# Performance work log

Measured on AMD Instinct MI355X. Metric: run time of the kernel, lower is better.

The kernel has to match this reference:

```python
import jax, jax.numpy as jnp
import numpy as np

EMBED = 1024
HEADS = 16
HEAD_DIM = EMBED // HEADS
FF = 4096
EPS = 1e-5


def layer_norm(x, g, b):
    mu = jnp.mean(x, axis=-1, keepdims=True)
    var = jnp.mean(jnp.square(x - mu), axis=-1, keepdims=True)
    return (x - mu) * jax.lax.rsqrt(var + EPS) * g + b


def setup_inputs() -> dict:
    key = jax.random.key(0)
    ks = jax.random.split(key, 16)
    s = 0.02
    x = jax.random.normal(ks[0], (4, 2048, EMBED), dtype=jnp.float32)
    d = {
        "x": x,
        "Wq": jax.random.normal(ks[1], (EMBED, EMBED), jnp.float32) * s,
        "bq": jnp.zeros((EMBED,), jnp.float32),
        "Wk": jax.random.normal(ks[2], (EMBED, EMBED), jnp.float32) * s,
        "bk": jnp.zeros((EMBED,), jnp.float32),
        "Wv": jax.random.normal(ks[3], (EMBED, EMBED), jnp.float32) * s,
        "bv": jnp.zeros((EMBED,), jnp.float32),
        "Wo": jax.random.normal(ks[4], (EMBED, EMBED), jnp.float32) * s,
        "bo": jnp.zeros((EMBED,), jnp.float32),
        "W1": jax.random.normal(ks[5], (EMBED, FF), jnp.float32) * s,
        "b1": jnp.zeros((FF,), jnp.float32),
        "W2": jax.random.normal(ks[6], (FF, EMBED), jnp.float32) * s,
        "b2": jnp.zeros((EMBED,), jnp.float32),
        "ln1_g": jnp.ones((EMBED,), jnp.float32),
        "ln1_b": jnp.zeros((EMBED,), jnp.float32),
        "ln2_g": jnp.ones((EMBED,), jnp.float32),
        "ln2_b": jnp.zeros((EMBED,), jnp.float32),
    }
    return d


def reference(x, Wq, bq, Wk, bk, Wv, bv, Wo, bo, W1, b1, W2, b2, ln1_g, ln1_b, ln2_g, ln2_b):
    B, S, E = x.shape
    scale = np.sqrt(HEAD_DIM).astype(np.float32)
    # project and split heads: (B, H, S, Dh)
    def heads(t):
        return t.reshape(B, S, HEADS, HEAD_DIM).transpose(0, 2, 1, 3)
    Q = heads(x @ Wq + bq)
    K = heads(x @ Wk + bk)
    V = heads(x @ Wv + bv)
    scores = jnp.einsum("bhqd,bhkd->bhqk", Q, K) / scale
    attn = jax.nn.softmax(scores, axis=-1)
    ctx = jnp.einsum("bhqk,bhkd->bhqd", attn, V)
    ctx = ctx.transpose(0, 2, 1, 3).reshape(B, S, E)
    attn_out = ctx @ Wo + bo
    x = layer_norm(x + attn_out, ln1_g, ln1_b)
    ff = jax.nn.relu(x @ W1 + b1) @ W2 + b2
    x = layer_norm(x + ff, ln2_g, ln2_b)
    return x
```

## Files before the change

kernel.cpp:

```cpp
#include <hip/hip_runtime.h>
#include <stdint.h>

typedef uint16_t u16;
typedef __bf16 bf16x8 __attribute__((ext_vector_type(8)));
typedef float f32x4 __attribute__((ext_vector_type(4)));

__device__ __forceinline__ float bf2f(u16 u) {
  union { uint32_t i; float f; } v; v.i = ((uint32_t)u) << 16; return v.f;
}
__device__ __forceinline__ u16 f2bf(float f) {
  union { float f; uint32_t i; } v; v.f = f;
  uint32_t r = v.i + 0x7fffu + ((v.i >> 16) & 1u);
  return (u16)(r >> 16);
}
__device__ __forceinline__ uint32_t pack2(float a, float b) {
  return (uint32_t)f2bf(a) | ((uint32_t)f2bf(b) << 16);
}
__device__ __forceinline__ void gll16(const u16* g, u16* l) {
  __builtin_amdgcn_global_load_lds((const __attribute__((address_space(1))) void*)g,
                                   (__attribute__((address_space(3))) void*)l, 16, 0, 0);
}

__global__ __launch_bounds__(256) void f32_to_bf16(
    const float* __restrict__ in, u16* __restrict__ out)
{
  int idx = blockIdx.x * 256 + threadIdx.x;
  float4 v = *(const float4*)(in + (size_t)idx * 4);
  uint2 o;
  o.x = pack2(v.x, v.y);
  o.y = pack2(v.z, v.w);
  *(uint2*)(out + (size_t)idx * 4) = o;
}

__global__ __launch_bounds__(256) void concat_bias(
    const float* __restrict__ a, const float* __restrict__ b,
    const float* __restrict__ c, float* __restrict__ o)
{
  int i = blockIdx.x * 256 + threadIdx.x;
  float v = (i < 1024) ? a[i] : ((i < 2048) ? b[i - 1024] : c[i - 2048]);
  o[i] = v;
}

__global__ __launch_bounds__(256) void transpose_f2b(
    const float* __restrict__ in, u16* __restrict__ out, int R, int C, int ldo)
{
  __shared__ u16 tile[32][33];
  int c0 = blockIdx.x * 32, r0 = blockIdx.y * 32;
  int x = threadIdx.x, y = threadIdx.y;
#pragma unroll
  for (int i = 0; i < 32; i += 8)
    tile[y + i][x] = f2bf(in[(size_t)(r0 + y + i) * C + (c0 + x)]);
  __syncthreads();
#pragma unroll
  for (int i = 0; i < 32; i += 8)
    out[(size_t)(c0 + y + i) * ldo + (r0 + x)] = tile[x][y + i];
}

__global__ __launch_bounds__(256) void transpose_v(
    const u16* __restrict__ src, u16* __restrict__ dst)
{
  __shared__ u16 tile[64][72];
  int kc = blockIdx.x;
  int bh = blockIdx.y;
  int b = bh >> 4, h = bh & 15;
  int t = threadIdx.x;
  int r = t >> 3;
  int c0 = (t & 7) * 8;
  const u16* s0 = src + ((size_t)(b * 2048 + kc * 64 + r) * 3072) + h * 64 + c0;
#pragma unroll
  for (int hh = 0; hh < 2; hh++)
    *(uint4*)(&tile[r + hh * 32][c0]) = *(const uint4*)(s0 + (size_t)hh * 32 * 3072);
  __syncthreads();
#pragma unroll
  for (int hh = 0; hh < 2; hh++) {
    int d = r + hh * 32;
    u16 vals[8];
#pragma unroll
    for (int p = 0; p < 8; p++) {
      int pos = c0 + p;
      int key = ((pos & 3) << 4) | ((pos >> 2) & 15);
      vals[p] = tile[key][d];
    }
    *(uint4*)(dst + ((size_t)bh * 64 + d) * 2048 + (size_t)kc * 64 + c0) = *(uint4*)vals;
  }
}

#define BM 128
#define BN 128
#define BK 64

__global__ __launch_bounds__(256, 2) void gemm_bt(
    const u16* __restrict__ A, const u16* __restrict__ BT,
    const float* __restrict__ bias, u16* __restrict__ C,
    int N, int K, int lda, int ldb, int ldc, int relu, int addC)
{
  __shared__ __align__(16) u16 As[BM][BK];
  __shared__ __align__(16) u16 Bs[BN][BK];
  int tid = threadIdx.x;
  int gx = gridDim.x;
  int id = blockIdx.y * gx + blockIdx.x;
  int cpx = (gx * gridDim.y) >> 3;
  int nid = (id & 7) * cpx + (id >> 3);
  int m0 = (nid / gx) * BM, n0 = (nid % gx) * BN;
  int wave = tid >> 6, lane = tid & 63;
  int quad = lane >> 4, tr = lane & 15;
  int wm = (wave >> 1) * 64, wn = (wave & 1) * 64;
  int tr7 = tr & 7;

  f32x4 zero = {0.f, 0.f, 0.f, 0.f};
  f32x4 acc[4][4];
#pragma unroll
  for (int i = 0; i < 4; i++)
#pragma unroll
    for (int j = 0; j < 4; j++) acc[i][j] = zero;

  int srow = tid >> 3;
  int sblk = (tid & 7) ^ (srow & 7);
  const u16* Abase = A  + (size_t)(m0 + srow) * lda + sblk * 8;
  const u16* Bbase = BT + (size_t)(n0 + srow) * ldb + sblk * 8;
  u16* la = &As[0][0] + tid * 8;
  u16* lb = &Bs[0][0] + tid * 8;

  for (int k0 = 0; k0 < K; k0 += BK) {
#pragma unroll
    for (int R = 0; R < 4; R++) {
      gll16(Abase + (size_t)(R * 32) * lda + k0, la + R * 2048);
      gll16(Bbase + (size_t)(R * 32) * ldb + k0, lb + R * 2048);
    }
    __syncthreads();
#pragma unroll
    for (int ks = 0; ks < 2; ks++) {
      bf16x8 af[4], bfr[4];
#pragma unroll
      for (int i = 0; i < 4; i++)
        af[i]  = *(const bf16x8*)(&As[wm + i*16 + tr][(((ks*4 + quad) ^ tr7)) * 8]);
#pragma unroll
      for (int j = 0; j < 4; j++)
        bfr[j] = *(const bf16x8*)(&Bs[wn + j*16 + tr][(((ks*4 + quad) ^ tr7)) * 8]);
#pragma unroll
      for (int i = 0; i < 4; i++)
#pragma unroll
        for (int j = 0; j < 4; j++)
          acc[i][j] = __builtin_amdgcn_mfma_f32_16x16x32_bf16(af[i], bfr[j], acc[i][j], 0, 0, 0);
    }
    __syncthreads();
  }

#pragma unroll
  for (int j = 0; j < 4; j++) {
    int n = n0 + wn + j*16 + tr;
    float bv = bias ? bias[n] : 0.f;
#pragma unroll
    for (int i = 0; i < 4; i++) {
      int mrow = m0 + wm + i*16 + quad*4;
#pragma unroll
      for (int r = 0; r < 4; r++) {
        size_t idx = (size_t)(mrow + r) * ldc + n;
        float v = acc[i][j][r] + bv;
        if (addC) v += bf2f(C[idx]);
        if (relu) v = v > 0.f ? v : 0.f;
        C[idx] = f2bf(v);
      }
    }
  }
}

__global__ __launch_bounds__(512, 4) void flash_attn(
    const u16* __restrict__ Qb, const u16* __restrict__ Kb,
    const u16* __restrict__ Vtg, u16* __restrict__ Ob, int ldqkv, int ldo)
{
  __shared__ __align__(16) u16 Ks[64][64];
  __shared__ __align__(16) u16 Vt[64][64];
  __shared__ __align__(16) u16 Ps[8][32][72];

  const int S = 2048;
  int tid = threadIdx.x;
  int wv = tid >> 6, lane = tid & 63;
  int quad = lane >> 4, tr = lane & 15;
  int tr7 = tr & 7;
  int id = blockIdx.y * 8 + blockIdx.x;
  int xcd = id & 7, sidx = id >> 3;
  int bh = xcd * 8 + (sidx & 7);
  int q0 = (sidx >> 3) * 256;
  int b = bh >> 4, h = bh & 15;
  int wq = wv * 32;
  size_t rowbase = (size_t)b * S;
  int colbase = h * 64;

  bf16x8 qf[2][2];
#pragma unroll
  for (int i = 0; i < 2; i++)
#pragma unroll
    for (int ks = 0; ks < 2; ks++)
      qf[i][ks] = *(const bf16x8*)(Qb + (rowbase + q0 + wq + i*16 + tr) * ldqkv
                                   + colbase + ks*32 + quad*8);

  f32x4 zero = {0.f, 0.f, 0.f, 0.f};
  f32x4 o[2][4];
  float lsum[2][4];
#pragma unroll
  for (int i = 0; i < 2; i++)
#pragma unroll
    for (int r = 0; r < 4; r++) lsum[i][r] = 0.f;
#pragma unroll
  for (int i = 0; i < 2; i++)
#pragma unroll
    for (int j = 0; j < 4; j++) o[i][j] = zero;

  const float sc = 0.125f;

  int srow = tid >> 3;
  int sblk = (tid & 7) ^ (srow & 7);
  const u16* kgbase = Kb + (rowbase + srow) * ldqkv + colbase + sblk * 8;
  const u16* vgbase = Vtg + ((size_t)bh * 64 + srow) * 2048 + sblk * 8;
  u16* kl = &Ks[0][0] + tid * 8;
  u16* vl = &Vt[0][0] + tid * 8;

  for (int kv0 = 0; kv0 < S; kv0 += 64) {
    gll16(kgbase + (size_t)kv0 * ldqkv, kl);
    gll16(vgbase + kv0, vl);
    __syncthreads();

    f32x4 s[2][4];
#pragma unroll
    for (int i = 0; i < 2; i++)
#pragma unroll
      for (int j = 0; j < 4; j++) s[i][j] = zero;
#pragma unroll
    for (int ks = 0; ks < 2; ks++) {
      bf16x8 kf[4];
#pragma unroll
      for (int j = 0; j < 4; j++)
        kf[j] = *(const bf16x8*)(&Ks[j*16 + tr][((ks*4 + quad) ^ tr7) * 8]);
#pragma unroll
      for (int i = 0; i < 2; i++)
#pragma unroll
        for (int j = 0; j < 4; j++)
          s[i][j] = __builtin_amdgcn_mfma_f32_16x16x32_bf16(qf[i][ks], kf[j], s[i][j], 0, 0, 0);
    }

#pragma unroll
    for (int i = 0; i < 2; i++) {
#pragma unroll
      for (int r = 0; r < 4; r++) {
        float p0 = __expf(s[i][0][r] * sc);
        float p1 = __expf(s[i][1][r] * sc);
        float p2 = __expf(s[i][2][r] * sc);
        float p3 = __expf(s[i][3][r] * sc);
        lsum[i][r] += (p0 + p1) + (p2 + p3);
        uint2 w;
        w.x = (__float_as_uint(p0) >> 16) | (__float_as_uint(p1) & 0xffff0000u);
        w.y = (__float_as_uint(p2) >> 16) | (__float_as_uint(p3) & 0xffff0000u);
        *(uint2*)(&Ps[wv][i*16 + quad*4 + r][tr*4]) = w;
      }
    }

#pragma unroll
    for (int ks = 0; ks < 2; ks++) {
      bf16x8 pf[2];
#pragma unroll
      for (int i = 0; i < 2; i++)
        pf[i] = *(const bf16x8*)(&Ps[wv][i*16 + tr][ks*32 + quad*8]);
#pragma unroll
      for (int jd = 0; jd < 4; jd++) {
        bf16x8 vf = *(const bf16x8*)(&Vt[jd*16 + tr][((ks*4 + quad) ^ tr7) * 8]);
#pragma unroll
        for (int i = 0; i < 2; i++)
          o[i][jd] = __builtin_amdgcn_mfma_f32_16x16x32_bf16(pf[i], vf, o[i][jd], 0, 0, 0);
      }
    }
    __syncthreads();
  }

#pragma unroll
  for (int i = 0; i < 2; i++) {
#pragma unroll
    for (int r = 0; r < 4; r++) {
      float l = lsum[i][r];
      l += __shfl_xor(l, 1, 64);
      l += __shfl_xor(l, 2, 64);
      l += __shfl_xor(l, 4, 64);
      l += __shfl_xor(l, 8, 64);
      float inv = 1.f / l;
      size_t qrow = rowbase + q0 + wq + i*16 + quad*4 + r;
#pragma unroll
      for (int jd = 0; jd < 4; jd++)
        Ob[qrow * ldo + colbase + jd*16 + tr] = f2bf(o[i][jd][r] * inv);
    }
  }
}

__global__ __launch_bounds__(256) void add_ln_a(
    const float* __restrict__ X, const u16* __restrict__ Rr,
    const float* __restrict__ G, const float* __restrict__ Bb,
    u16* __restrict__ Y)
{
  int row = blockIdx.x;
  int tid = threadIdx.x;
  __shared__ float sbuf[4], qbuf[4];
  float4 xv = *(const float4*)(X + (size_t)row * 1024 + tid * 4);
  uint2 ru = *(const uint2*)(Rr + (size_t)row * 1024 + tid * 4);
  const u16* rs = (const u16*)&ru;
  const float* xs = (const float*)&xv;
  float v[4];
  float s = 0.f, q = 0.f;
#pragma unroll
  for (int e = 0; e < 4; e++) {
    float a = xs[e] + bf2f(rs[e]);
    v[e] = a; s += a; q += a * a;
  }
#pragma unroll
  for (int off = 1; off < 64; off <<= 1) {
    s += __shfl_xor(s, off, 64);
    q += __shfl_xor(q, off, 64);
  }
  if ((tid & 63) == 0) { sbuf[tid >> 6] = s; qbuf[tid >> 6] = q; }
  __syncthreads();
  s = sbuf[0] + sbuf[1] + sbuf[2] + sbuf[3];
  q = qbuf[0] + qbuf[1] + qbuf[2] + qbuf[3];
  float mu  = s * (1.f / 1024.f);
  float var = q * (1.f / 1024.f) - mu * mu;
  float inv = rsqrtf(var + 1e-5f);
#pragma unroll
  for (int e = 0; e < 4; e++) {
    int col = tid * 4 + e;
    float yv = (v[e] - mu) * inv * G[col] + Bb[col];
    Y[(size_t)row * 1024 + col] = f2bf(yv);
  }
}

__global__ __launch_bounds__(256) void add_ln_b(
    const u16* __restrict__ X, const u16* __restrict__ Rr,
    const float* __restrict__ G, const float* __restrict__ Bb,
    float* __restrict__ Y)
{
  int row = blockIdx.x;
  int tid = threadIdx.x;
  __shared__ float sbuf[4], qbuf[4];
  uint2 xu = *(const uint2*)(X  + (size_t)row * 1024 + tid * 4);
  uint2 ru = *(const uint2*)(Rr + (size_t)row * 1024 + tid * 4);
  const u16* xs = (const u16*)&xu;
  const u16* rs = (const u16*)&ru;
  float v[4];
  float s = 0.f, q = 0.f;
#pragma unroll
  for (int e = 0; e < 4; e++) {
    float a = bf2f(xs[e]) + bf2f(rs[e]);
    v[e] = a; s += a; q += a * a;
  }
#pragma unroll
  for (int off = 1; off < 64; off <<= 1) {
    s += __shfl_xor(s, off, 64);
    q += __shfl_xor(q, off, 64);
  }
  if ((tid & 63) == 0) { sbuf[tid >> 6] = s; qbuf[tid >> 6] = q; }
  __syncthreads();
  s = sbuf[0] + sbuf[1] + sbuf[2] + sbuf[3];
  q = qbuf[0] + qbuf[1] + qbuf[2] + qbuf[3];
  float mu  = s * (1.f / 1024.f);
  float var = q * (1.f / 1024.f) - mu * mu;
  float inv = rsqrtf(var + 1e-5f);
  float4 yv;
  float* yp = (float*)&yv;
#pragma unroll
  for (int e = 0; e < 4; e++) {
    int col = tid * 4 + e;
    yp[e] = (v[e] - mu) * inv * G[col] + Bb[col];
  }
  *(float4*)(Y + (size_t)row * 1024 + tid * 4) = yv;
}

extern "C" void kernel_launch(void* const* d_in, const int* in_sizes, int n_in,
                              void* d_out, int out_size, void* d_ws, size_t ws_size,
                              hipStream_t stream) {
  const float* x   = (const float*)d_in[0];
  const float* Wq  = (const float*)d_in[1];
  const float* bq  = (const float*)d_in[2];
  const float* Wk  = (const float*)d_in[3];
  const float* bk  = (const float*)d_in[4];
  const float* Wv  = (const float*)d_in[5];
  const float* bv  = (const float*)d_in[6];
  const float* Wo  = (const float*)d_in[7];
  const float* bo  = (const float*)d_in[8];
  const float* W1  = (const float*)d_in[9];
  const float* b1  = (const float*)d_in[10];
  const float* W2  = (const float*)d_in[11];
  const float* b2  = (const float*)d_in[12];
  const float* g1  = (const float*)d_in[13];
  const float* be1 = (const float*)d_in[14];
  const float* g2  = (const float*)d_in[15];
  const float* be2 = (const float*)d_in[16];
  float* out = (float*)d_out;
  u16* ws  = (u16*)d_ws;

  const int Nrow = 8192, E = 1024, FFd = 4096;
  const size_t M1 = 1048576;
  u16* xb     = ws;
  u16* WqkvT  = ws + 8  * M1;
  u16* WoT    = ws + 11 * M1;
  u16* W1T    = ws + 12 * M1;
  u16* W2T    = ws + 16 * M1;
  u16* QKV    = ws + 20 * M1;
  u16* Vtg    = ws;
  u16* X1     = ws;
  u16* F2     = ws + 20 * M1;
  float* bqkv = (float*)d_out;
  u16*  AO    = (u16*)d_out;
  u16*  Hc    = (u16*)d_out;

  dim3 tb(256);
  dim3 tt(32, 8);
  f32_to_bf16<<<dim3(8192), tb, 0, stream>>>(x, xb);
  transpose_f2b<<<dim3(E/32,  E/32),  tt, 0, stream>>>(Wq, WqkvT,        E,   E,   E);
  transpose_f2b<<<dim3(E/32,  E/32),  tt, 0, stream>>>(Wk, WqkvT + 1*M1, E,   E,   E);
  transpose_f2b<<<dim3(E/32,  E/32),  tt, 0, stream>>>(Wv, WqkvT + 2*M1, E,   E,   E);
  transpose_f2b<<<dim3(E/32,  E/32),  tt, 0, stream>>>(Wo, WoT,          E,   E,   E);
  transpose_f2b<<<dim3(FFd/32,E/32),  tt, 0, stream>>>(W1, W1T,          E,   FFd, E);
  transpose_f2b<<<dim3(E/32,  FFd/32),tt, 0, stream>>>(W2, W2T,          FFd, E,   FFd);
  concat_bias<<<dim3(12), tb, 0, stream>>>(bq, bk, bv, bqkv);

  gemm_bt<<<dim3(24, Nrow/BM), tb, 0, stream>>>(xb, WqkvT, bqkv, QKV,
                                                3072, E, E, E, 3072, 0, 0);
  transpose_v<<<dim3(32, 64), tb, 0, stream>>>(QKV + 2048, Vtg);
  flash_attn<<<dim3(8, 64), dim3(512), 0, stream>>>(QKV, QKV + 1024, Vtg,
                                                    QKV + 2048, 3072, 3072);
  gemm_bt<<<dim3(8, Nrow/BM), tb, 0, stream>>>(QKV + 2048, WoT, bo, AO,
                                               E, E, 3072, E, E, 0, 0);
  add_ln_a<<<dim3(Nrow), tb, 0, stream>>>(x, AO, g1, be1, X1);

  for (int c = 0; c < 2; c++) {
    gemm_bt<<<dim3(16, Nrow/BM), tb, 0, stream>>>(
        X1, W1T + (size_t)c * 2048 * E, b1 + c * 2048, Hc,
        2048, E, E, E, 2048, 1, 0);
    gemm_bt<<<dim3(8, Nrow/BM), tb, 0, stream>>>(
        Hc, W2T + (size_t)c * 2048, (c == 0 ? b2 : (const float*)nullptr), F2,
        E, 2048, 2048, FFd, E, 0, (c == 0 ? 0 : 1));
  }

  add_ln_b<<<dim3(Nrow), tb, 0, stream>>>(X1, F2, g2, be2, out);
}
```

Baseline: 533.5 us.

## Double-buffer K/V tiles in flash attention and use exp2 with byte-perm packing

Flash attention now keeps two LDS buffers each for K and V. The next tile's global-to-LDS load is issued before computing on the current tile, so memory latency overlaps the MFMA work and one barrier per iteration is dropped. The softmax exponent uses the hardware exp2 with a prescaled log2(e)/8 constant, and bf16 truncation packing uses a single v_perm instead of shift/mask. The change doubles K/V LDS usage, which may affect occupancy under the 4-blocks-per-CU launch bound.

```diff
diff --git a/kernel.cpp b/kernel.cpp
--- a/kernel.cpp
+++ b/kernel.cpp
@@ -169,8 +169,8 @@
     const u16* __restrict__ Qb, const u16* __restrict__ Kb,
     const u16* __restrict__ Vtg, u16* __restrict__ Ob, int ldqkv, int ldo)
 {
-  __shared__ __align__(16) u16 Ks[64][64];
-  __shared__ __align__(16) u16 Vt[64][64];
+  __shared__ __align__(16) u16 Ks[2][64][64];
+  __shared__ __align__(16) u16 Vt[2][64][64];
   __shared__ __align__(16) u16 Ps[8][32][72];
 
   const int S = 2048;
@@ -207,19 +207,27 @@
 #pragma unroll
     for (int j = 0; j < 4; j++) o[i][j] = zero;
 
-  const float sc = 0.125f;
+  const float SCL = 0.18033688011112042f;
 
   int srow = tid >> 3;
   int sblk = (tid & 7) ^ (srow & 7);
   const u16* kgbase = Kb + (rowbase + srow) * ldqkv + colbase + sblk * 8;
   const u16* vgbase = Vtg + ((size_t)bh * 64 + srow) * 2048 + sblk * 8;
-  u16* kl = &Ks[0][0] + tid * 8;
-  u16* vl = &Vt[0][0] + tid * 8;
+
+  const u16* krd = &Ks[0][0][0];
+  const u16* vrd = &Vt[0][0][0];
+  u16* kwr = &Ks[1][0][0] + tid * 8;
+  u16* vwr = &Vt[1][0][0] + tid * 8;
+
+  gll16(kgbase, &Ks[0][0][0] + tid * 8);
+  gll16(vgbase, &Vt[0][0][0] + tid * 8);
+  __syncthreads();
 
   for (int kv0 = 0; kv0 < S; kv0 += 64) {
-    gll16(kgbase + (size_t)kv0 * ldqkv, kl);
-    gll16(vgbase + kv0, vl);
-    __syncthreads();
+    if (kv0 + 64 < S) {
+      gll16(kgbase + (size_t)(kv0 + 64) * ldqkv, kwr);
+      gll16(vgbase + (kv0 + 64), vwr);
+    }
 
     f32x4 s[2][4];
 #pragma unroll
@@ -231,7 +239,7 @@
       bf16x8 kf[4];
 #pragma unroll
       for (int j = 0; j < 4; j++)
-        kf[j] = *(const bf16x8*)(&Ks[j*16 + tr][((ks*4 + quad) ^ tr7) * 8]);
+        kf[j] = *(const bf16x8*)(krd + (size_t)(j*16 + tr) * 64 + ((ks*4 + quad) ^ tr7) * 8);
 #pragma unroll
       for (int i = 0; i < 2; i++)
 #pragma unroll
@@ -243,14 +251,14 @@
     for (int i = 0; i < 2; i++) {
 #pragma unroll
       for (int r = 0; r < 4; r++) {
-        float p0 = __expf(s[i][0][r] * sc);
-        float p1 = __expf(s[i][1][r] * sc);
-        float p2 = __expf(s[i][2][r] * sc);
-        float p3 = __expf(s[i][3][r] * sc);
+        float p0 = __builtin_amdgcn_exp2f(s[i][0][r] * SCL);
+        float p1 = __builtin_amdgcn_exp2f(s[i][1][r] * SCL);
+        float p2 = __builtin_amdgcn_exp2f(s[i][2][r] * SCL);
+        float p3 = __builtin_amdgcn_exp2f(s[i][3][r] * SCL);
         lsum[i][r] += (p0 + p1) + (p2 + p3);
         uint2 w;
-        w.x = (__float_as_uint(p0) >> 16) | (__float_as_uint(p1) & 0xffff0000u);
-        w.y = (__float_as_uint(p2) >> 16) | (__float_as_uint(p3) & 0xffff0000u);
+        w.x = __builtin_amdgcn_perm(__float_as_uint(p1), __float_as_uint(p0), 0x07060302u);
+        w.y = __builtin_amdgcn_perm(__float_as_uint(p3), __float_as_uint(p2), 0x07060302u);
         *(uint2*)(&Ps[wv][i*16 + quad*4 + r][tr*4]) = w;
       }
     }
@@ -263,13 +271,16 @@
         pf[i] = *(const bf16x8*)(&Ps[wv][i*16 + tr][ks*32 + quad*8]);
 #pragma unroll
       for (int jd = 0; jd < 4; jd++) {
-        bf16x8 vf = *(const bf16x8*)(&Vt[jd*16 + tr][((ks*4 + quad) ^ tr7) * 8]);
+        bf16x8 vf = *(const bf16x8*)(vrd + (size_t)(jd*16 + tr) * 64 + ((ks*4 + quad) ^ tr7) * 8);
 #pragma unroll
         for (int i = 0; i < 2; i++)
           o[i][jd] = __builtin_amdgcn_mfma_f32_16x16x32_bf16(pf[i], vf, o[i][jd], 0, 0, 0);
       }
     }
+
     __syncthreads();
+    const u16* t1 = krd; krd = kwr - tid * 8; kwr = (u16*)t1 + tid * 8;
+    const u16* t2 = vrd; vrd = vwr - tid * 8; vwr = (u16*)t2 + tid * 8;
   }
 
 #pragma unroll
```

Result: slower. 547.1 us (+2.5%).

## Double-buffer K/V in flash attention and keep P in registers via transposed MFMA

Applied to the files above, without the earlier changes.

The attention kernel now double-buffers K and V tiles in LDS, prefetching the next 64-key block while computing the current one. It computes S transposed (K as the A operand), so the bf16-packed probabilities can go straight into the PV MFMA through byte permutes instead of a round trip through shared memory. It also uses exp2 with a folded scale, and switches to 256-thread blocks covering 128 queries with twice as many blocks. The V transpose key permutation is changed to match the new P register layout, and the GEMM launch bound is raised to 3 blocks per CU, which may cause register spills.

```diff
diff --git a/kernel.cpp b/kernel.cpp
--- a/kernel.cpp
+++ b/kernel.cpp
@@ -78,7 +78,7 @@
 #pragma unroll
     for (int p = 0; p < 8; p++) {
       int pos = c0 + p;
-      int key = ((pos & 3) << 4) | ((pos >> 2) & 15);
+      int key = (pos & 0x23) | ((pos & 4) << 2) | ((pos >> 1) & 0x0C);
       vals[p] = tile[key][d];
     }
     *(uint4*)(dst + ((size_t)bh * 64 + d) * 2048 + (size_t)kc * 64 + c0) = *(uint4*)vals;
@@ -89,7 +89,7 @@
 #define BN 128
 #define BK 64
 
-__global__ __launch_bounds__(256, 2) void gemm_bt(
+__global__ __launch_bounds__(256, 3) void gemm_bt(
     const u16* __restrict__ A, const u16* __restrict__ BT,
     const float* __restrict__ bias, u16* __restrict__ C,
     int N, int K, int lda, int ldb, int ldc, int relu, int addC)
@@ -165,23 +165,21 @@
   }
 }
 
-__global__ __launch_bounds__(512, 4) void flash_attn(
+__global__ __launch_bounds__(256, 4) void flash_attn(
     const u16* __restrict__ Qb, const u16* __restrict__ Kb,
     const u16* __restrict__ Vtg, u16* __restrict__ Ob, int ldqkv, int ldo)
 {
-  __shared__ __align__(16) u16 Ks[64][64];
-  __shared__ __align__(16) u16 Vt[64][64];
-  __shared__ __align__(16) u16 Ps[8][32][72];
+  __shared__ __align__(16) u16 Ks[2][4096];
+  __shared__ __align__(16) u16 Vt[2][4096];
 
   const int S = 2048;
   int tid = threadIdx.x;
   int wv = tid >> 6, lane = tid & 63;
-  int quad = lane >> 4, tr = lane & 15;
-  int tr7 = tr & 7;
-  int id = blockIdx.y * 8 + blockIdx.x;
+  int quad = lane >> 4, tr = lane & 15, tr7 = tr & 7;
+  int id = blockIdx.y * 16 + blockIdx.x;
   int xcd = id & 7, sidx = id >> 3;
   int bh = xcd * 8 + (sidx & 7);
-  int q0 = (sidx >> 3) * 256;
+  int q0 = (sidx >> 3) * 128;
   int b = bh >> 4, h = bh & 15;
   int wq = wv * 32;
   size_t rowbase = (size_t)b * S;
@@ -197,92 +195,115 @@
 
   f32x4 zero = {0.f, 0.f, 0.f, 0.f};
   f32x4 o[2][4];
-  float lsum[2][4];
+  float lsum[2] = {0.f, 0.f};
 #pragma unroll
   for (int i = 0; i < 2; i++)
 #pragma unroll
-    for (int r = 0; r < 4; r++) lsum[i][r] = 0.f;
-#pragma unroll
-  for (int i = 0; i < 2; i++)
-#pragma unroll
     for (int j = 0; j < 4; j++) o[i][j] = zero;
 
-  const float sc = 0.125f;
+  const float SCL = 0.18033688011112042f;
 
   int srow = tid >> 3;
   int sblk = (tid & 7) ^ (srow & 7);
-  const u16* kgbase = Kb + (rowbase + srow) * ldqkv + colbase + sblk * 8;
-  const u16* vgbase = Vtg + ((size_t)bh * 64 + srow) * 2048 + sblk * 8;
-  u16* kl = &Ks[0][0] + tid * 8;
-  u16* vl = &Vt[0][0] + tid * 8;
+  const u16* kg = Kb + (rowbase + srow) * ldqkv + colbase + sblk * 8;
+  const u16* vg = Vtg + ((size_t)bh * 64 + srow) * 2048 + sblk * 8;
+  size_t kstep32 = (size_t)32 * ldqkv;
+
+  gll16(kg,            &Ks[0][0] + tid * 8);
+  gll16(kg + kstep32,  &Ks[0][0] + 2048 + tid * 8);
+  gll16(vg,            &Vt[0][0] + tid * 8);
+  gll16(vg + 32*2048,  &Vt[0][0] + 2048 + tid * 8);
+  __syncthreads();
 
   for (int kv0 = 0; kv0 < S; kv0 += 64) {
-    gll16(kgbase + (size_t)kv0 * ldqkv, kl);
-    gll16(vgbase + kv0, vl);
-    __syncthreads();
-
-    f32x4 s[2][4];
-#pragma unroll
-    for (int i = 0; i < 2; i++)
-#pragma unroll
-      for (int j = 0; j < 4; j++) s[i][j] = zero;
+    int cur = (kv0 >> 6) & 1;
+    if (kv0 + 64 < S) {
+      const u16* kn = kg + (size_t)(kv0 + 64) * ldqkv;
+      const u16* vn = vg + (kv0 + 64);
+      u16* kd = &Ks[cur ^ 1][0] + tid * 8;
+      u16* vd = &Vt[cur ^ 1][0] + tid * 8;
+      gll16(kn,           kd);
+      gll16(kn + kstep32, kd + 2048);
+      gll16(vn,           vd);
+      gll16(vn + 32*2048, vd + 2048);
+    }
+
+    const u16* kb = &Ks[cur][0];
+    const u16* vb = &Vt[cur][0];
+
+    f32x4 s2[4][2];
+#pragma unroll
+    for (int j = 0; j < 4; j++)
+#pragma unroll
+      for (int i = 0; i < 2; i++) s2[j][i] = zero;
 #pragma unroll
     for (int ks = 0; ks < 2; ks++) {
       bf16x8 kf[4];
 #pragma unroll
       for (int j = 0; j < 4; j++)
-        kf[j] = *(const bf16x8*)(&Ks[j*16 + tr][((ks*4 + quad) ^ tr7) * 8]);
-#pragma unroll
-      for (int i = 0; i < 2; i++)
-#pragma unroll
-        for (int j = 0; j < 4; j++)
-          s[i][j] = __builtin_amdgcn_mfma_f32_16x16x32_bf16(qf[i][ks], kf[j], s[i][j], 0, 0, 0);
-    }
-
-#pragma unroll
-    for (int i = 0; i < 2; i++) {
-#pragma unroll
-      for (int r = 0; r < 4; r++) {
-        float p0 = __expf(s[i][0][r] * sc);
-        float p1 = __expf(s[i][1][r] * sc);
-        float p2 = __expf(s[i][2][r] * sc);
-        float p3 = __expf(s[i][3][r] * sc);
-        lsum[i][r] += (p0 + p1) + (p2 + p3);
-        uint2 w;
-        w.x = (__float_as_uint(p0) >> 16) | (__float_as_uint(p1) & 0xffff0000u);
-        w.y = (__float_as_uint(p2) >> 16) | (__float_as_uint(p3) & 0xffff0000u);
-        *(uint2*)(&Ps[wv][i*16 + quad*4 + r][tr*4]) = w;
+        kf[j] = *(const bf16x8*)(kb + (size_t)(j*16 + tr) * 64 + ((ks*4 + quad) ^ tr7) * 8);
+#pragma unroll
+      for (int j = 0; j < 4; j++)
+#pragma unroll
+        for (int i = 0; i < 2; i++)
+          s2[j][i] = __builtin_amdgcn_mfma_f32_16x16x32_bf16(kf[j], qf[i][ks], s2[j][i], 0, 0, 0);
+    }
+
+#pragma unroll
+    for (int j = 0; j < 4; j++) {
+#pragma unroll
+      for (int i = 0; i < 2; i++) {
+        float p0 = __builtin_amdgcn_exp2f(s2[j][i][0] * SCL);
+        float p1 = __builtin_amdgcn_exp2f(s2[j][i][1] * SCL);
+        float p2 = __builtin_amdgcn_exp2f(s2[j][i][2] * SCL);
+        float p3 = __builtin_amdgcn_exp2f(s2[j][i][3] * SCL);
+        lsum[i] += (p0 + p1) + (p2 + p3);
+        s2[j][i][0] = p0; s2[j][i][1] = p1; s2[j][i][2] = p2; s2[j][i][3] = p3;
       }
     }
 
 #pragma unroll
     for (int ks = 0; ks < 2; ks++) {
-      bf16x8 pf[2];
-#pragma unroll
-      for (int i = 0; i < 2; i++)
-        pf[i] = *(const bf16x8*)(&Ps[wv][i*16 + tr][ks*32 + quad*8]);
+      bf16x8 pa[2];
+#pragma unroll
+      for (int i = 0; i < 2; i++) {
+        union { uint32_t w[4]; bf16x8 v; } u;
+        u.w[0] = __builtin_amdgcn_perm(__float_as_uint(s2[2*ks][i][1]),
+                                       __float_as_uint(s2[2*ks][i][0]), 0x07060302u);
+        u.w[1] = __builtin_amdgcn_perm(__float_as_uint(s2[2*ks][i][3]),
+                                       __float_as_uint(s2[2*ks][i][2]), 0x07060302u);
+        u.w[2] = __builtin_amdgcn_perm(__float_as_uint(s2[2*ks+1][i][1]),
+                                       __float_as_uint(s2[2*ks+1][i][0]), 0x07060302u);
+        u.w[3] = __builtin_amdgcn_perm(__float_as_uint(s2[2*ks+1][i][3]),
+                                       __float_as_uint(s2[2*ks+1][i][2]), 0x07060302u);
+        pa[i] = u.v;
+      }
 #pragma unroll
       for (int jd = 0; jd < 4; jd++) {
-        bf16x8 vf = *(const bf16x8*)(&Vt[jd*16 + tr][((ks*4 + quad) ^ tr7) * 8]);
+        bf16x8 vf = *(const bf16x8*)(vb + (size_t)(jd*16 + tr) * 64 + ((ks*4 + quad) ^ tr7) * 8);
 #pragma unroll
         for (int i = 0; i < 2; i++)
-          o[i][jd] = __builtin_amdgcn_mfma_f32_16x16x32_bf16(pf[i], vf, o[i][jd], 0, 0, 0);
+          o[i][jd] = __builtin_amdgcn_mfma_f32_16x16x32_bf16(pa[i], vf, o[i][jd], 0, 0, 0);
       }
     }
+
     __syncthreads();
   }
 
 #pragma unroll
   for (int i = 0; i < 2; i++) {
+    float l = lsum[i];
+    l += __shfl_xor(l, 16, 64);
+    l += __shfl_xor(l, 32, 64);
+    lsum[i] = l;
+  }
+#pragma unroll
+  for (int i = 0; i < 2; i++) {
 #pragma unroll
     for (int r = 0; r < 4; r++) {
-      float l = lsum[i][r];
-      l += __shfl_xor(l, 1, 64);
-      l += __shfl_xor(l, 2, 64);
-      l += __shfl_xor(l, 4, 64);
-      l += __shfl_xor(l, 8, 64);
-      float inv = 1.f / l;
-      size_t qrow = rowbase + q0 + wq + i*16 + quad*4 + r;
+      int qr = quad * 4 + r;
+      float inv = 1.f / __shfl(lsum[i], qr, 64);
+      size_t qrow = rowbase + q0 + wq + i*16 + qr;
 #pragma unroll
       for (int jd = 0; jd < 4; jd++)
         Ob[qrow * ldo + colbase + jd*16 + tr] = f2bf(o[i][jd][r] * inv);
@@ -422,8 +443,8 @@
   gemm_bt<<<dim3(24, Nrow/BM), tb, 0, stream>>>(xb, WqkvT, bqkv, QKV,
                                                 3072, E, E, E, 3072, 0, 0);
   transpose_v<<<dim3(32, 64), tb, 0, stream>>>(QKV + 2048, Vtg);
-  flash_attn<<<dim3(8, 64), dim3(512), 0, stream>>>(QKV, QKV + 1024, Vtg,
-                                                    QKV + 2048, 3072, 3072);
+  flash_attn<<<dim3(16, 64), dim3(256), 0, stream>>>(QKV, QKV + 1024, Vtg,
+                                                     QKV + 2048, 3072, 3072);
   gemm_bt<<<dim3(8, Nrow/BM), tb, 0, stream>>>(QKV + 2048, WoT, bo, AO,
                                                E, E, 3072, E, E, 0, 0);
   add_ln_a<<<dim3(Nrow), tb, 0, stream>>>(x, AO, g1, be1, X1);
```

Result: no change. 529.1 us (-0.8%).
